# Kernel optimization log

Measured on AMD Instinct MI355X. Metric: run time of the kernel, lower is better.

## Reference

```python
import jax, jax.numpy as jnp
import numpy as np

N = 100_000          # NEURON_COUNT (scaled)
INPUT_SIZE = 1024    # input neurons occupy indices [0, INPUT_SIZE)
OUTPUT_SIZE = 256    # output neurons occupy indices [N-OUTPUT_SIZE, N)
E = 10_000_000       # SYNAPSE_RATIO * N
STEPS = 3


def setup_inputs() -> dict:
    key = jax.random.key(0)
    k1, k2, k3, k4, k5 = jax.random.split(key, 5)
    x = jax.random.normal(k1, (INPUT_SIZE,), dtype=jnp.float32)
    synapse_weights = jax.random.normal(k2, (E,), dtype=jnp.float32)
    neuron_biases = jax.random.normal(k3, (N - INPUT_SIZE,), dtype=jnp.float32)
    synapse_src = jax.random.randint(k4, (E,), 0, N, dtype=jnp.int64) if jax.config.jax_enable_x64 else jax.random.randint(k4, (E,), 0, N, dtype=jnp.int32)
    synapse_dst = jax.random.randint(k5, (E,), 0, N, dtype=jnp.int64) if jax.config.jax_enable_x64 else jax.random.randint(k5, (E,), 0, N, dtype=jnp.int32)
    return {
        "x": x,
        "synapse_weights": synapse_weights,
        "neuron_biases": neuron_biases,
        "synapse_src": synapse_src,
        "synapse_dst": synapse_dst,
    }


def reference(x, synapse_weights, neuron_biases, synapse_src, synapse_dst):
    # Initial state: zeros everywhere, inputs injected at the first INPUT_SIZE slots.
    v = jnp.zeros((N,), dtype=x.dtype).at[:INPUT_SIZE].set(x.reshape(-1))
    # tanh applied to all neurons except outputs (last OUTPUT_SIZE indices)
    tanh_mask = jnp.arange(N) < (N - OUTPUT_SIZE)
    for _ in range(STEPS):
        # vectorized gather-multiply-scatter: next[to] += v[from] * w  (one segment_sum)
        msg = v[synapse_src] * synapse_weights                       # [E]
        nxt = jax.ops.segment_sum(msg, synapse_dst, num_segments=N)  # [N]
        # biases added to all non-input neurons
        nxt = nxt.at[INPUT_SIZE:].add(neuron_biases)
        # tanh everywhere except output neurons
        v = jnp.where(tanh_mask, jnp.tanh(nxt), nxt)
    return v[N - OUTPUT_SIZE:]
```

## Files before the change

### kernel.cpp

```cpp
#include <hip/hip_runtime.h>

#define N_NEURONS   100000
#define INPUT_SIZE  1024
#define OUTPUT_SIZE 256
#define E_SYN       10000000
#define STEPS       3

#define RANGES      8
#define BIN         12500
#define SCAT_BLK    1024
#define CBLK        64
#define RG          8
#define RSL         (CBLK / RG)
#define CAP         1280000
#define STG_CAP     128
#define VEC4        (E_SYN / 4)

#define CHK         2048
#define NCH         4883
#define PITER       (CHK / (64 * 4))
#define HIST_GRID   ((NCH + 3) / 4)
#define PART_GRID   ((NCH + 1) / 2)

__global__ void init_state(const float* __restrict__ x, float* __restrict__ v) {
    int i = blockIdx.x * blockDim.x + threadIdx.x;
    if (i < N_NEURONS) v[i] = (i < INPUT_SIZE) ? x[i] : 0.0f;
}

__global__ __launch_bounds__(256) void hist_kernel(const int* __restrict__ dst,
                                                   int* __restrict__ hist) {
    const int lane  = threadIdx.x & 63;
    const int wv    = threadIdx.x >> 6;
    const int chunk = blockIdx.x * 4 + wv;
    if (chunk >= NCH) return;
    const long beg = (long)chunk * CHK;
    const int4* dst4 = (const int4*)dst;
    int h = 0;
    for (int it = 0; it < PITER; ++it) {
        long e  = beg + (long)(it * 64 + lane) * 4;
        bool ok = (e < E_SYN);
        int4 d4 = ok ? dst4[e >> 2] : make_int4(0, 0, 0, 0);
        unsigned long long okm = __ballot(ok);
        int rk[4] = {d4.x / BIN, d4.y / BIN, d4.z / BIN, d4.w / BIN};
#pragma unroll
        for (int k = 0; k < 4; ++k) {
            unsigned long long b0 = __ballot(rk[k] & 1);
            unsigned long long b1 = __ballot(rk[k] & 2);
            unsigned long long b2 = __ballot(rk[k] & 4);
            unsigned long long m = ((lane & 1) ? b0 : ~b0) &
                                   ((lane & 2) ? b1 : ~b1) &
                                   ((lane & 4) ? b2 : ~b2) & okm;
            h += __popcll(m);
        }
    }
    if (lane < RANGES) hist[(size_t)lane * NCH + chunk] = h;
}

__global__ __launch_bounds__(1024) void scan_kernel(const int* __restrict__ hist,
                                                    int* __restrict__ bases,
                                                    int* __restrict__ gcur) {
    const int r = blockIdx.x;
    const int t = threadIdx.x;
    const int lane = t & 63;
    const int wv   = t >> 6;
    int vals[5];
    int s = 0;
#pragma unroll
    for (int j = 0; j < 5; ++j) {
        int idx = t * 5 + j;
        int vv  = (idx < NCH) ? hist[(size_t)r * NCH + idx] : 0;
        vals[j] = vv;
        s += vv;
    }
    int x = s;
#pragma unroll
    for (int d = 1; d < 64; d <<= 1) {
        int y = __shfl_up(x, d, 64);
        if (lane >= d) x += y;
    }
    __shared__ int wsum[16];
    if (lane == 63) wsum[wv] = x;
    __syncthreads();
    if (wv == 0) {
        int y = (lane < 16) ? wsum[lane] : 0;
        int z = y;
#pragma unroll
        for (int d = 1; d < 16; d <<= 1) {
            int u = __shfl_up(z, d, 64);
            if (lane >= d) z += u;
        }
        if (lane < 16) wsum[lane] = z - y;
    }
    __syncthreads();
    int run = (x - s) + wsum[wv];
#pragma unroll
    for (int j = 0; j < 5; ++j) {
        int idx = t * 5 + j;
        if (idx < NCH) bases[(size_t)r * NCH + idx] = r * CAP + run;
        run += vals[j];
    }
    if (t == 1023) gcur[r] = run;
}

__global__ __launch_bounds__(128) void partition_kernel(
        const float* __restrict__ w,
        const int*   __restrict__ src,
        const int*   __restrict__ dst,
        const int*   __restrict__ bases,
        int2* __restrict__ recs) {
    __shared__ int2 stg[2][RANGES][STG_CAP];
    const int lane  = threadIdx.x & 63;
    const int wv    = threadIdx.x >> 6;
    const int chunk = blockIdx.x * 2 + wv;
    if (chunk >= NCH) return;
    const unsigned long long ltmask = (1ull << lane) - 1ull;

    int cur = 0, wrr = 0, flr = 0;
    if (lane < RANGES) cur = bases[(size_t)lane * NCH + chunk];

    const long beg = (long)chunk * CHK;
    const int4* dst4 = (const int4*)dst;
    const int4* src4 = (const int4*)src;
    const int4* wq4  = (const int4*)w;

    for (int it = 0; it < PITER; ++it) {
        long e  = beg + (long)(it * 64 + lane) * 4;
        bool ok = (e < E_SYN);
        int4 d4 = ok ? dst4[e >> 2] : make_int4(0, 0, 0, 0);
        int4 s4 = ok ? src4[e >> 2] : make_int4(0, 0, 0, 0);
        int4 q4 = ok ? wq4[e >> 2]  : make_int4(0, 0, 0, 0);
        unsigned long long okm = __ballot(ok);
        int dd[4] = {d4.x, d4.y, d4.z, d4.w};
        int ss[4] = {s4.x, s4.y, s4.z, s4.w};
        int qq[4] = {q4.x, q4.y, q4.z, q4.w};
#pragma unroll
        for (int k = 0; k < 4; ++k) {
            int d = dd[k];
            int r = d / BIN;
            unsigned long long b0 = __ballot(r & 1);
            unsigned long long b1 = __ballot(r & 2);
            unsigned long long b2 = __ballot(r & 4);
            unsigned long long mym = ((r & 1) ? b0 : ~b0) &
                                     ((r & 2) ? b1 : ~b1) &
                                     ((r & 4) ? b2 : ~b2) & okm;
            int rank  = __popcll(mym & ltmask);
            int wslot = __shfl(wrr, r, 64);
            int slot  = (wslot + rank) & (STG_CAP - 1);
            if (ok) stg[wv][r][slot] = make_int2((ss[k] << 14) | (d - r * BIN), qq[k]);
            unsigned long long mm = ((lane & 1) ? b0 : ~b0) &
                                    ((lane & 2) ? b1 : ~b1) &
                                    ((lane & 4) ? b2 : ~b2) & okm;
            wrr += __popcll(mm);
            unsigned long long fb = __ballot(wrr - flr >= 64) & 0xFFull;
            while (fb) {
                int rr = __ffsll((long long)fb) - 1;
                fb &= fb - 1;
                int gpos = __shfl(cur, rr, 64);
                int f0   = __shfl(flr, rr, 64) & (STG_CAP - 1);
                int2 rec = stg[wv][rr][f0 + lane];
                recs[(size_t)gpos + lane] = rec;
                if (lane == rr) { flr += 64; cur += 64; }
            }
        }
    }
#pragma unroll
    for (int rr = 0; rr < RANGES; ++rr) {
        int wt = __shfl(wrr, rr, 64);
        int ft = __shfl(flr, rr, 64);
        int pend = wt - ft;
        if (pend > 0) {
            int gpos = __shfl(cur, rr, 64);
            if (lane < pend)
                recs[(size_t)gpos + lane] = stg[wv][rr][(ft & (STG_CAP - 1)) + lane];
        }
    }
}

__global__ __launch_bounds__(SCAT_BLK) void scatter_sorted(
        const int2* __restrict__ recs,
        const int*  __restrict__ gcur,
        const float* __restrict__ v,
        float* __restrict__ partials) {
    __shared__ float bins[BIN];
    const int r = blockIdx.x / CBLK;
    const int c = blockIdx.x % CBLK;
    for (int j = threadIdx.x; j < BIN; j += SCAT_BLK) bins[j] = 0.0f;
    __syncthreads();

    const int cnt   = gcur[r];
    const int npair = cnt >> 1;
    const int4* base4 = (const int4*)(recs + (size_t)r * CAP);
    const int stride = CBLK * SCAT_BLK;
    int u = c * SCAT_BLK + threadIdx.x;
    for (; u + 3 * stride < npair; u += 4 * stride) {
        int4 a = base4[u];
        int4 b = base4[u + stride];
        int4 e = base4[u + 2 * stride];
        int4 f = base4[u + 3 * stride];
        float va0 = v[a.x >> 14];
        float va1 = v[a.z >> 14];
        float vb0 = v[b.x >> 14];
        float vb1 = v[b.z >> 14];
        float ve0 = v[e.x >> 14];
        float ve1 = v[e.z >> 14];
        float vf0 = v[f.x >> 14];
        float vf1 = v[f.z >> 14];
        atomicAdd(&bins[a.x & 16383], va0 * __int_as_float(a.y));
        atomicAdd(&bins[a.z & 16383], va1 * __int_as_float(a.w));
        atomicAdd(&bins[b.x & 16383], vb0 * __int_as_float(b.y));
        atomicAdd(&bins[b.z & 16383], vb1 * __int_as_float(b.w));
        atomicAdd(&bins[e.x & 16383], ve0 * __int_as_float(e.y));
        atomicAdd(&bins[e.z & 16383], ve1 * __int_as_float(e.w));
        atomicAdd(&bins[f.x & 16383], vf0 * __int_as_float(f.y));
        atomicAdd(&bins[f.z & 16383], vf1 * __int_as_float(f.w));
    }
    for (; u < npair; u += stride) {
        int4 a = base4[u];
        atomicAdd(&bins[a.x & 16383], v[a.x >> 14] * __int_as_float(a.y));
        atomicAdd(&bins[a.z & 16383], v[a.z >> 14] * __int_as_float(a.w));
    }
    if ((cnt & 1) && c == 0 && threadIdx.x == 0) {
        int2 p = recs[(size_t)r * CAP + cnt - 1];
        atomicAdd(&bins[p.x & 16383], v[p.x >> 14] * __int_as_float(p.y));
    }
    __syncthreads();
    float* o = partials + (size_t)(r * CBLK + c) * BIN;
    for (int j = threadIdx.x; j < BIN; j += SCAT_BLK) o[j] = bins[j];
}

__global__ void reduce_fused(const float* __restrict__ partials,
                             const float* __restrict__ bias,
                             float* __restrict__ v,
                             float* __restrict__ out,
                             int write_out) {
    int i4 = 4 * (blockIdx.x * blockDim.x + threadIdx.x);
    if (i4 >= N_NEURONS) return;
    const int r = i4 / BIN;
    const int j = i4 - r * BIN;
    const float* base = partials + (size_t)(r * CBLK) * BIN + j;
    float4 tot = {0.f, 0.f, 0.f, 0.f};
#pragma unroll 2
    for (int g = 0; g < RG; ++g) {
        float4 a = {0.f, 0.f, 0.f, 0.f};
#pragma unroll
        for (int cc = 0; cc < RSL; ++cc) {
            float4 p = *(const float4*)(base + (size_t)(g * RSL + cc) * BIN);
            a.x += p.x; a.y += p.y; a.z += p.z; a.w += p.w;
        }
        tot.x += a.x; tot.y += a.y; tot.z += a.z; tot.w += a.w;
    }
    float av[4] = {tot.x, tot.y, tot.z, tot.w};
#pragma unroll
    for (int k = 0; k < 4; ++k) {
        int i = i4 + k;
        float val = av[k] + ((i >= INPUT_SIZE) ? bias[i - INPUT_SIZE] : 0.0f);
        float nv  = (i < N_NEURONS - OUTPUT_SIZE) ? tanhf(val) : val;
        v[i] = nv;
        if (write_out && i >= N_NEURONS - OUTPUT_SIZE)
            out[i - (N_NEURONS - OUTPUT_SIZE)] = val;
    }
}

__global__ void scatter_binned(const float* __restrict__ w,
                               const int*   __restrict__ src,
                               const int*   __restrict__ dst,
                               const float* __restrict__ v,
                               float*       __restrict__ partials,
                               int C) {
    __shared__ float bins[BIN];
    const int r = blockIdx.x / C;
    const int c = blockIdx.x % C;
    const int lo = r * BIN;
    const int hi = lo + BIN;
    for (int j = threadIdx.x; j < BIN; j += blockDim.x) bins[j] = 0.0f;
    __syncthreads();
    const int4*   src4 = (const int4*)src;
    const int4*   dst4 = (const int4*)dst;
    const float4* w4v  = (const float4*)w;
    const int stride = C * blockDim.x;
    for (int u = c * blockDim.x + threadIdx.x; u < VEC4; u += stride) {
        const int4   s4 = src4[u];
        const int4   d4 = dst4[u];
        const float4 wv = w4v[u];
        int   s[4] = {s4.x, s4.y, s4.z, s4.w};
        int   d[4] = {d4.x, d4.y, d4.z, d4.w};
        float ww[4] = {wv.x, wv.y, wv.z, wv.w};
#pragma unroll
        for (int k = 0; k < 4; ++k)
            if (d[k] >= lo && d[k] < hi)
                atomicAdd(&bins[d[k] - lo], v[s[k]] * ww[k]);
    }
    __syncthreads();
    float* o = partials + ((size_t)(r * C + c)) * BIN;
    for (int j = threadIdx.x; j < BIN; j += blockDim.x) o[j] = bins[j];
}
__global__ void reduce_update_fb(const float* __restrict__ partials,
                                 const float* __restrict__ bias,
                                 float* __restrict__ v,
                                 float* __restrict__ out,
                                 int C, int write_out) {
    int i4 = 4 * (blockIdx.x * blockDim.x + threadIdx.x);
    if (i4 >= N_NEURONS) return;
    const int r = i4 / BIN;
    const int j = i4 - r * BIN;
    const float* base = partials + ((size_t)r * C) * BIN + j;
    float4 acc = {0.f, 0.f, 0.f, 0.f};
    for (int c = 0; c < C; ++c) {
        float4 p = *(const float4*)(base + (size_t)c * BIN);
        acc.x += p.x; acc.y += p.y; acc.z += p.z; acc.w += p.w;
    }
    float av[4] = {acc.x, acc.y, acc.z, acc.w};
#pragma unroll
    for (int k = 0; k < 4; ++k) {
        int i = i4 + k;
        float val = av[k] + ((i >= INPUT_SIZE) ? bias[i - INPUT_SIZE] : 0.0f);
        float nv  = (i < N_NEURONS - OUTPUT_SIZE) ? tanhf(val) : val;
        v[i] = nv;
        if (write_out && i >= N_NEURONS - OUTPUT_SIZE)
            out[i - (N_NEURONS - OUTPUT_SIZE)] = val;
    }
}

extern "C" void kernel_launch(void* const* d_in, const int* in_sizes, int n_in,
                              void* d_out, int out_size, void* d_ws, size_t ws_size,
                              hipStream_t stream) {
    const float* x    = (const float*)d_in[0];
    const float* w    = (const float*)d_in[1];
    const float* bias = (const float*)d_in[2];
    const int*   src  = (const int*)d_in[3];
    const int*   dst  = (const int*)d_in[4];
    float* out = (float*)d_out;

    const int blk = 256;
    const int grid_n   = (N_NEURONS + blk - 1) / blk;
    const int red_grid = (N_NEURONS / 4 + blk - 1) / blk;

    float* v        = (float*)d_ws;
    float* partials = v + N_NEURONS;
    int*   hist     = (int*)(partials + (size_t)RANGES * CBLK * BIN);
    int*   bases    = hist + (size_t)RANGES * NCH;
    int2*  recs     = (int2*)(bases + (size_t)RANGES * NCH);
    int*   gcur     = (int*)(recs + (size_t)RANGES * CAP);
    size_t need = (size_t)((char*)(gcur + RANGES) - (char*)d_ws);

    if (ws_size >= need) {
        init_state<<<grid_n, blk, 0, stream>>>(x, v);
        hist_kernel<<<HIST_GRID, 256, 0, stream>>>(dst, hist);
        scan_kernel<<<RANGES, 1024, 0, stream>>>(hist, bases, gcur);
        partition_kernel<<<PART_GRID, 128, 0, stream>>>(w, src, dst, bases, recs);
        for (int s = 0; s < STEPS; ++s) {
            scatter_sorted<<<RANGES * CBLK, SCAT_BLK, 0, stream>>>(
                recs, gcur, v, partials);
            reduce_fused<<<red_grid, blk, 0, stream>>>(
                partials, bias, v, out, s == STEPS - 1 ? 1 : 0);
        }
    } else {
        long C = (long)(ws_size / 4 / N_NEURONS) - 1;
        if (C > 64) C = 64;
        if (C < 1) C = 1;
        float* part_fb = v + N_NEURONS;
        init_state<<<grid_n, blk, 0, stream>>>(x, v);
        for (int s = 0; s < STEPS; ++s) {
            scatter_binned<<<RANGES * (int)C, SCAT_BLK, 0, stream>>>(
                w, src, dst, v, part_fb, (int)C);
            reduce_update_fb<<<red_grid, blk, 0, stream>>>(
                part_fb, bias, v, out, (int)C, s == STEPS - 1 ? 1 : 0);
        }
    }
}
```

Baseline: 378.1 us.

## Drop LDS staging in partition, write records directly with smaller chunks

The partition kernel no longer stages records in shared memory and flushes them in 64-record bursts. Each lane now writes its record straight to its global position, computed from a per-range cursor plus its ballot rank. Chunks are halved to 1024 edges, so there are twice as many histogram entries, and blocks grow to four waves. This removes LDS traffic and the flush loop, but the global writes become scattered across 8 ranges, which may hurt write coalescing.

```diff
diff --git a/kernel.cpp b/kernel.cpp
--- a/kernel.cpp
+++ b/kernel.cpp
@@ -13,14 +13,15 @@
 #define RG          8
 #define RSL         (CBLK / RG)
 #define CAP         1280000
-#define STG_CAP     128
 #define VEC4        (E_SYN / 4)
 
-#define CHK         2048
-#define NCH         4883
-#define PITER       (CHK / (64 * 4))
-#define HIST_GRID   ((NCH + 3) / 4)
-#define PART_GRID   ((NCH + 1) / 2)
+#define CHK         1024
+#define NCH         9766
+#define PITER       (CHK / 256)
+#define PW          4
+#define HIST_GRID   ((NCH + PW - 1) / PW)
+#define PART_GRID   ((NCH + PW - 1) / PW)
+#define SCJ         ((NCH + 1023) / 1024)
 
 __global__ void init_state(const float* __restrict__ x, float* __restrict__ v) {
     int i = blockIdx.x * blockDim.x + threadIdx.x;
@@ -31,13 +32,13 @@
                                                    int* __restrict__ hist) {
     const int lane  = threadIdx.x & 63;
     const int wv    = threadIdx.x >> 6;
-    const int chunk = blockIdx.x * 4 + wv;
+    const int chunk = blockIdx.x * PW + wv;
     if (chunk >= NCH) return;
-    const long beg = (long)chunk * CHK;
+    const int beg = chunk * CHK;
     const int4* dst4 = (const int4*)dst;
     int h = 0;
     for (int it = 0; it < PITER; ++it) {
-        long e  = beg + (long)(it * 64 + lane) * 4;
+        int e   = beg + (it * 64 + lane) * 4;
         bool ok = (e < E_SYN);
         int4 d4 = ok ? dst4[e >> 2] : make_int4(0, 0, 0, 0);
         unsigned long long okm = __ballot(ok);
@@ -63,11 +64,11 @@
     const int t = threadIdx.x;
     const int lane = t & 63;
     const int wv   = t >> 6;
-    int vals[5];
+    int vals[SCJ];
     int s = 0;
 #pragma unroll
-    for (int j = 0; j < 5; ++j) {
-        int idx = t * 5 + j;
+    for (int j = 0; j < SCJ; ++j) {
+        int idx = t * SCJ + j;
         int vv  = (idx < NCH) ? hist[(size_t)r * NCH + idx] : 0;
         vals[j] = vv;
         s += vv;
@@ -94,41 +95,41 @@
     __syncthreads();
     int run = (x - s) + wsum[wv];
 #pragma unroll
-    for (int j = 0; j < 5; ++j) {
-        int idx = t * 5 + j;
+    for (int j = 0; j < SCJ; ++j) {
+        int idx = t * SCJ + j;
         if (idx < NCH) bases[(size_t)r * NCH + idx] = r * CAP + run;
         run += vals[j];
     }
     if (t == 1023) gcur[r] = run;
 }
 
-__global__ __launch_bounds__(128) void partition_kernel(
+__global__ __launch_bounds__(256) void partition_kernel(
         const float* __restrict__ w,
         const int*   __restrict__ src,
         const int*   __restrict__ dst,
         const int*   __restrict__ bases,
         int2* __restrict__ recs) {
-    __shared__ int2 stg[2][RANGES][STG_CAP];
     const int lane  = threadIdx.x & 63;
     const int wv    = threadIdx.x >> 6;
-    const int chunk = blockIdx.x * 2 + wv;
+    const int chunk = blockIdx.x * PW + wv;
     if (chunk >= NCH) return;
     const unsigned long long ltmask = (1ull << lane) - 1ull;
 
-    int cur = 0, wrr = 0, flr = 0;
+    int cur = 0;
     if (lane < RANGES) cur = bases[(size_t)lane * NCH + chunk];
 
-    const long beg = (long)chunk * CHK;
+    const int beg = chunk * CHK;
     const int4* dst4 = (const int4*)dst;
     const int4* src4 = (const int4*)src;
     const int4* wq4  = (const int4*)w;
 
     for (int it = 0; it < PITER; ++it) {
-        long e  = beg + (long)(it * 64 + lane) * 4;
+        int e   = beg + (it * 64 + lane) * 4;
         bool ok = (e < E_SYN);
-        int4 d4 = ok ? dst4[e >> 2] : make_int4(0, 0, 0, 0);
-        int4 s4 = ok ? src4[e >> 2] : make_int4(0, 0, 0, 0);
-        int4 q4 = ok ? wq4[e >> 2]  : make_int4(0, 0, 0, 0);
+        int idx = e >> 2;
+        int4 d4 = ok ? dst4[idx] : make_int4(0, 0, 0, 0);
+        int4 s4 = ok ? src4[idx] : make_int4(0, 0, 0, 0);
+        int4 q4 = ok ? wq4[idx]  : make_int4(0, 0, 0, 0);
         unsigned long long okm = __ballot(ok);
         int dd[4] = {d4.x, d4.y, d4.z, d4.w};
         int ss[4] = {s4.x, s4.y, s4.z, s4.w};
@@ -143,35 +144,14 @@
             unsigned long long mym = ((r & 1) ? b0 : ~b0) &
                                      ((r & 2) ? b1 : ~b1) &
                                      ((r & 4) ? b2 : ~b2) & okm;
-            int rank  = __popcll(mym & ltmask);
-            int wslot = __shfl(wrr, r, 64);
-            int slot  = (wslot + rank) & (STG_CAP - 1);
-            if (ok) stg[wv][r][slot] = make_int2((ss[k] << 14) | (d - r * BIN), qq[k]);
+            int rank = __popcll(mym & ltmask);
+            int gpos = __shfl(cur, r, 64) + rank;
+            if (ok) recs[(size_t)gpos] =
+                make_int2((ss[k] << 14) | (d - r * BIN), qq[k]);
             unsigned long long mm = ((lane & 1) ? b0 : ~b0) &
                                     ((lane & 2) ? b1 : ~b1) &
                                     ((lane & 4) ? b2 : ~b2) & okm;
-            wrr += __popcll(mm);
-            unsigned long long fb = __ballot(wrr - flr >= 64) & 0xFFull;
-            while (fb) {
-                int rr = __ffsll((long long)fb) - 1;
-                fb &= fb - 1;
-                int gpos = __shfl(cur, rr, 64);
-                int f0   = __shfl(flr, rr, 64) & (STG_CAP - 1);
-                int2 rec = stg[wv][rr][f0 + lane];
-                recs[(size_t)gpos + lane] = rec;
-                if (lane == rr) { flr += 64; cur += 64; }
-            }
-        }
-    }
-#pragma unroll
-    for (int rr = 0; rr < RANGES; ++rr) {
-        int wt = __shfl(wrr, rr, 64);
-        int ft = __shfl(flr, rr, 64);
-        int pend = wt - ft;
-        if (pend > 0) {
-            int gpos = __shfl(cur, rr, 64);
-            if (lane < pend)
-                recs[(size_t)gpos + lane] = stg[wv][rr][(ft & (STG_CAP - 1)) + lane];
+            cur += __popcll(mm);
         }
     }
 }
@@ -347,7 +327,7 @@
         init_state<<<grid_n, blk, 0, stream>>>(x, v);
         hist_kernel<<<HIST_GRID, 256, 0, stream>>>(dst, hist);
         scan_kernel<<<RANGES, 1024, 0, stream>>>(hist, bases, gcur);
-        partition_kernel<<<PART_GRID, 128, 0, stream>>>(w, src, dst, bases, recs);
+        partition_kernel<<<PART_GRID, 256, 0, stream>>>(w, src, dst, bases, recs);
         for (int s = 0; s < STEPS; ++s) {
             scatter_sorted<<<RANGES * CBLK, SCAT_BLK, 0, stream>>>(
                 recs, gcur, v, partials);
```

Result: no change. 384.5 us (+1.7%).
